# Optimization experiments

Hardware: AMD Instinct MI355X
Metric: run time of the kernel (lower is better)

The kernel has to match this reference:

```python
import jax, jax.numpy as jnp
import numpy as np

C_M, C_Z, H, CH = 256, 128, 8, 32
EPS = 1e-5

def layer_norm(x, g, b):
    mu = jnp.mean(x, axis=-1, keepdims=True)
    var = jnp.mean(jnp.square(x - mu), axis=-1, keepdims=True)
    return (x - mu) * jax.lax.rsqrt(var + EPS) * g + b

def setup_inputs() -> dict:
    key = jax.random.key(0)
    ks = jax.random.split(key, 12)
    B, N, L = 1, 256, 256
    m = jax.random.normal(ks[0], (B, N, L, C_M), dtype=jnp.float32)
    z = jax.random.normal(ks[1], (B, L, L, C_Z), dtype=jnp.float32)
    msa_mask = jax.random.randint(ks[2], (B, N, L), 0, 2, dtype=jnp.int32)
    s = 0.02
    return {
        "m": m, "z": z, "msa_mask": msa_mask,
        "ln_m_g": jnp.ones((C_M,), jnp.float32), "ln_m_b": jnp.zeros((C_M,), jnp.float32),
        "ln_z_g": jnp.ones((C_Z,), jnp.float32), "ln_z_b": jnp.zeros((C_Z,), jnp.float32),
        "Wq": s * jax.random.normal(ks[3], (C_M, H * CH), jnp.float32),
        "Wk": s * jax.random.normal(ks[4], (C_M, H * CH), jnp.float32),
        "Wv": s * jax.random.normal(ks[5], (C_M, H * CH), jnp.float32),
        "Wb": s * jax.random.normal(ks[6], (C_Z, H), jnp.float32),
        "Wg": s * jax.random.normal(ks[7], (C_M, H * CH), jnp.float32),
        "bg": jnp.zeros((H * CH,), jnp.float32),
        "Wo": s * jax.random.normal(ks[8], (H * CH, C_M), jnp.float32),
        "bo": jnp.zeros((C_M,), jnp.float32),
    }

def reference(m, z, msa_mask, ln_m_g, ln_m_b, ln_z_g, ln_z_b,
              Wq, Wk, Wv, Wb, Wg, bg, Wo, bo):
    B, N, L, _ = m.shape
    mn = layer_norm(m, ln_m_g, ln_m_b)          # [B,N,L,c_m]
    zn = layer_norm(z, ln_z_g, ln_z_b)          # [B,L,L,c_z]
    q = (mn @ Wq).reshape(B, N, L, H, CH)
    k = (mn @ Wk).reshape(B, N, L, H, CH)
    v = (mn @ Wv).reshape(B, N, L, H, CH)
    pair_bias = zn @ Wb                          # [B,L,L,H]
    logits = jnp.einsum('bnihc,bnjhc->bnhij', q, k) / np.sqrt(CH).astype(np.float32)
    logits = logits + jnp.transpose(pair_bias, (0, 3, 1, 2))[:, None]  # [B,1,H,i,j]
    # key mask over j: [B,N,1,1,L]
    logits = jnp.where(msa_mask[:, :, None, None, :] == 0, jnp.float32(-1e9), logits)
    attn = jax.nn.softmax(logits, axis=-1)
    out = jnp.einsum('bnhij,bnjhc->bnihc', attn, v)
    gate = jax.nn.sigmoid(mn @ Wg + bg).reshape(B, N, L, H, CH)
    out = (out * gate).reshape(B, N, L, H * CH)
    out = out @ Wo + bo
    out = out * msa_mask[..., None].astype(out.dtype)
    return out
```

## Files before the change

### kernel.cpp

```cpp
#include <hip/hip_runtime.h>

typedef unsigned short ushort_t;
typedef unsigned int uint_t;
typedef __attribute__((ext_vector_type(8))) short bf16x8;
typedef __attribute__((ext_vector_type(4))) float f32x4;

#define EPSV 1e-5f
#define LOG2E 1.4426950408889634f
#define QSC (0.17677669529663687f * LOG2E)

__device__ __forceinline__ float u2f(uint_t x) { return __builtin_bit_cast(float, x); }
__device__ __forceinline__ uint_t f2u(float x) { return __builtin_bit_cast(uint_t, x); }
__device__ __forceinline__ float bflo(uint_t u) { return u2f(u << 16); }
__device__ __forceinline__ float bfhi(uint_t u) { return u2f(u & 0xFFFF0000u); }
__device__ __forceinline__ ushort_t f2bf(float f) {
    uint_t x = f2u(f);
    x += 0x7FFFu + ((x >> 16) & 1u);
    return (ushort_t)(x >> 16);
}
__device__ __forceinline__ uint_t cvtpk(float lo, float hi) {
    uint_t r;
    asm("v_cvt_pk_bf16_f32 %0, %1, %2" : "=v"(r) : "v"(lo), "v"(hi));
    return r;
}
__device__ __forceinline__ float exp2v(float x) {
    float r;
    asm("v_exp_f32 %0, %1" : "=v"(r) : "v"(x));
    return r;
}
__device__ __forceinline__ float rcpv(float x) {
    float r;
    asm("v_rcp_f32 %0, %1" : "=v"(r) : "v"(x));
    return r;
}
__device__ __forceinline__ f32x4 mfma16(bf16x8 a, bf16x8 b, f32x4 c) {
    return __builtin_amdgcn_mfma_f32_16x16x32_bf16(a, b, c, 0, 0, 0);
}
__device__ __forceinline__ float wsum(float v) {
#pragma unroll
    for (int m = 32; m >= 1; m >>= 1) v += __shfl_xor(v, m, 64);
    return v;
}

#define NB_LN 16384
#define NB_PB 1024
__global__ __launch_bounds__(256) void k_pre(const float* __restrict__ m,
                                             const float* __restrict__ ln_m_g,
                                             const float* __restrict__ ln_m_b,
                                             const float* __restrict__ z,
                                             const float* __restrict__ ln_z_g,
                                             const float* __restrict__ ln_z_b,
                                             const float* __restrict__ Wb,
                                             const float* __restrict__ Wq, const float* __restrict__ Wk,
                                             const float* __restrict__ Wv, const float* __restrict__ Wg,
                                             const float* __restrict__ Wo,
                                             ushort_t* __restrict__ mn,
                                             float* __restrict__ pb,
                                             ushort_t* __restrict__ wtT, ushort_t* __restrict__ woT) {
    __shared__ float wb_lds[1024];
    const int bid = blockIdx.x, t = threadIdx.x;

    if (bid < NB_LN) {
        const int lane = t & 63;
        const int row  = bid * 4 + (t >> 6);
        const float4 x = *(const float4*)(m + (size_t)row * 256 + lane * 4);
        const float mu = wsum(x.x + x.y + x.z + x.w) * (1.f / 256.f);
        const float dx = x.x - mu, dy = x.y - mu, dz = x.z - mu, dw = x.w - mu;
        const float var = wsum(dx * dx + dy * dy + dz * dz + dw * dw) * (1.f / 256.f);
        const float rs = rsqrtf(var + EPSV);
        const float4 gg = *(const float4*)(ln_m_g + lane * 4);
        const float4 bb = *(const float4*)(ln_m_b + lane * 4);
        ushort4 o;
        o.x = f2bf(dx * rs * gg.x + bb.x);
        o.y = f2bf(dy * rs * gg.y + bb.y);
        o.z = f2bf(dz * rs * gg.z + bb.z);
        o.w = f2bf(dw * rs * gg.w + bb.w);
        *(ushort4*)(mn + (size_t)row * 256 + lane * 4) = o;
    } else if (bid < NB_LN + NB_PB) {
        const int pbid = bid - NB_LN;
        const int w = t >> 6, l = t & 63;
        const int l16 = l & 15, gq = l >> 4;
        *(float4*)&wb_lds[t * 4] = *(const float4*)(Wb + t * 4);
        __syncthreads();

        const int row = pbid * 64 + w * 16 + l16;
        const float* zr = z + (size_t)row * 128;
        float v[32];
        float s1 = 0.f, s2 = 0.f;
#pragma unroll
        for (int ks = 0; ks < 4; ++ks) {
            const float4 a0 = *(const float4*)(zr + ks * 32 + gq * 8);
            const float4 a1 = *(const float4*)(zr + ks * 32 + gq * 8 + 4);
            v[ks * 8 + 0] = a0.x; v[ks * 8 + 1] = a0.y; v[ks * 8 + 2] = a0.z; v[ks * 8 + 3] = a0.w;
            v[ks * 8 + 4] = a1.x; v[ks * 8 + 5] = a1.y; v[ks * 8 + 6] = a1.z; v[ks * 8 + 7] = a1.w;
        }
#pragma unroll
        for (int j = 0; j < 32; ++j) { s1 += v[j]; s2 += v[j] * v[j]; }
        s1 += __shfl_xor(s1, 16, 64); s1 += __shfl_xor(s1, 32, 64);
        s2 += __shfl_xor(s2, 16, 64); s2 += __shfl_xor(s2, 32, 64);
        const float mu = s1 * (1.f / 128.f);
        const float var = s2 * (1.f / 128.f) - mu * mu;
        const float rs = rsqrtf(var + EPSV);

        f32x4 acc = (f32x4){0.f, 0.f, 0.f, 0.f};
#pragma unroll
        for (int ks = 0; ks < 4; ++ks) {
            const float4 g0 = *(const float4*)(ln_z_g + ks * 32 + gq * 8);
            const float4 g1 = *(const float4*)(ln_z_g + ks * 32 + gq * 8 + 4);
            const float4 b0 = *(const float4*)(ln_z_b + ks * 32 + gq * 8);
            const float4 b1 = *(const float4*)(ln_z_b + ks * 32 + gq * 8 + 4);
            const float xn0 = (v[ks * 8 + 0] - mu) * rs * g0.x + b0.x;
            const float xn1 = (v[ks * 8 + 1] - mu) * rs * g0.y + b0.y;
            const float xn2 = (v[ks * 8 + 2] - mu) * rs * g0.z + b0.z;
            const float xn3 = (v[ks * 8 + 3] - mu) * rs * g0.w + b0.w;
            const float xn4 = (v[ks * 8 + 4] - mu) * rs * g1.x + b1.x;
            const float xn5 = (v[ks * 8 + 5] - mu) * rs * g1.y + b1.y;
            const float xn6 = (v[ks * 8 + 6] - mu) * rs * g1.z + b1.z;
            const float xn7 = (v[ks * 8 + 7] - mu) * rs * g1.w + b1.w;
            uint4 pk;
            pk.x = cvtpk(xn0, xn1); pk.y = cvtpk(xn2, xn3);
            pk.z = cvtpk(xn4, xn5); pk.w = cvtpk(xn6, xn7);
            const bf16x8 af = __builtin_bit_cast(bf16x8, pk);
            ushort_t wf[8];
#pragma unroll
            for (int j = 0; j < 8; ++j)
                wf[j] = (l16 < 8) ? f2bf(wb_lds[(ks * 32 + gq * 8 + j) * 8 + l16]) : (ushort_t)0;
            const bf16x8 bf_ = *(const bf16x8*)wf;
            acc = mfma16(af, bf_, acc);
        }
        if (l16 < 8) {
            const int orow = pbid * 64 + w * 16 + gq * 4;
            f32x4 o;
            o[0] = acc[0] * LOG2E; o[1] = acc[1] * LOG2E;
            o[2] = acc[2] * LOG2E; o[3] = acc[3] * LOG2E;
            *(f32x4*)(pb + (size_t)l16 * 65536 + orow) = o;
        }
    } else {
        const int k = bid - (NB_LN + NB_PB);
        const int h = t >> 5, c = t & 31;
        wtT[(size_t)(h * 128 +   0 + c) * 256 + k] = f2bf(Wq[k * 256 + t]);
        wtT[(size_t)(h * 128 +  32 + c) * 256 + k] = f2bf(Wk[k * 256 + t]);
        wtT[(size_t)(h * 128 +  64 + c) * 256 + k] = f2bf(Wv[k * 256 + t]);
        wtT[(size_t)(h * 128 +  96 + c) * 256 + k] = f2bf(Wg[k * 256 + t]);
        woT[(size_t)t * 256 + k] = f2bf(Wo[k * 256 + t]);
    }
}

__global__ __launch_bounds__(256, 1) void k_attn(const ushort_t* __restrict__ mn,
                                                 const ushort_t* __restrict__ wtT,
                                                 const float* __restrict__ pb,
                                                 const int* __restrict__ msa_mask,
                                                 const float* __restrict__ bg,
                                                 ushort_t* __restrict__ ao) {
    __shared__ ushort_t k_s[256 * 40];
    __shared__ ushort_t qp_s[256 * 40];
    __shared__ ushort_t vT[32 * 264];
    __shared__ ushort_t gT[32 * 264];
    __shared__ float maskb[256];

    const int t = threadIdx.x;
    const int n = blockIdx.x & 255, h = blockIdx.x >> 8;
    const int w = t >> 6, l = t & 63;
    const int l16 = l & 15, g = l >> 4;

    maskb[t] = msa_mask[n * 256 + t] ? 0.f : -1.5e9f;
    const float bg0 = bg[h * 32 + l16];
    const float bg1 = bg[h * 32 + 16 + l16];

    const ushort_t* mb = mn + (size_t)n * 65536;
    const ushort_t* wb = wtT + (size_t)h * 128 * 256;

#pragma unroll
    for (int chalf = 0; chalf < 2; ++chalf) {
        f32x4 acc[4][4];
#pragma unroll
        for (int rt = 0; rt < 4; ++rt)
#pragma unroll
            for (int ct = 0; ct < 4; ++ct) acc[rt][ct] = (f32x4){0.f, 0.f, 0.f, 0.f};

#pragma unroll
        for (int ks = 0; ks < 8; ++ks) {
            bf16x8 a[4], b[4];
#pragma unroll
            for (int rt = 0; rt < 4; ++rt)
                a[rt] = *(const bf16x8*)(mb + (size_t)(w * 64 + rt * 16 + l16) * 256 + ks * 32 + g * 8);
#pragma unroll
            for (int ct = 0; ct < 4; ++ct)
                b[ct] = *(const bf16x8*)(wb + (size_t)(chalf * 64 + ct * 16 + l16) * 256 + ks * 32 + g * 8);
#pragma unroll
            for (int rt = 0; rt < 4; ++rt)
#pragma unroll
                for (int ct = 0; ct < 4; ++ct)
                    acc[rt][ct] = mfma16(a[rt], b[ct], acc[rt][ct]);
        }
#pragma unroll
        for (int ct = 0; ct < 4; ++ct) {
            const int mat = chalf * 2 + (ct >> 1);
            const int cc = (ct & 1) * 16 + l16;
#pragma unroll
            for (int rt = 0; rt < 4; ++rt) {
                const int i0 = w * 64 + rt * 16 + g * 4;
                const f32x4 v = acc[rt][ct];
                if (mat == 0) {
#pragma unroll
                    for (int r = 0; r < 4; ++r) qp_s[(i0 + r) * 40 + cc] = f2bf(v[r] * QSC);
                } else if (mat == 1) {
#pragma unroll
                    for (int r = 0; r < 4; ++r) k_s[(i0 + r) * 40 + cc] = f2bf(v[r]);
                } else if (mat == 2) {
                    const uint_t lo = cvtpk(v[0], v[1]);
                    const uint_t hi = cvtpk(v[2], v[3]);
                    *(uint2*)(vT + cc * 264 + i0) = make_uint2(lo, hi);
                } else {
                    const float bgc = (ct & 1) ? bg1 : bg0;
                    float gt[4];
#pragma unroll
                    for (int r = 0; r < 4; ++r)
                        gt[r] = rcpv(1.f + exp2v(-(v[r] + bgc) * LOG2E));
                    const uint_t lo = cvtpk(gt[0], gt[1]);
                    const uint_t hi = cvtpk(gt[2], gt[3]);
                    *(uint2*)(gT + cc * 264 + i0) = make_uint2(lo, hi);
                }
            }
        }
    }
    __syncthreads();

    bf16x8 bq[4];
#pragma unroll
    for (int it = 0; it < 4; ++it)
        bq[it] = *(const bf16x8*)&qp_s[(w * 64 + it * 16 + l16) * 40 + g * 8];
    ushort_t* p_w = qp_s + w * 64 * 40;

    const float* pbh = pb + (size_t)h * 65536;
    f32x4 oT[2][4];
#pragma unroll
    for (int ct = 0; ct < 2; ++ct)
#pragma unroll
        for (int it = 0; it < 4; ++it) oT[ct][it] = (f32x4){0.f, 0.f, 0.f, 0.f};
    float lsum[4] = {0.f, 0.f, 0.f, 0.f};

    bf16x8 ak[2], av[2];
    f32x4 pc0[4], pc1[4];
#pragma unroll
    for (int jt = 0; jt < 2; ++jt)
        ak[jt] = *(const bf16x8*)&k_s[(jt * 16 + l16) * 40 + g * 8];
#pragma unroll
    for (int ct = 0; ct < 2; ++ct)
        av[ct] = *(const bf16x8*)&vT[(ct * 16 + l16) * 264 + g * 8];
#pragma unroll
    for (int it = 0; it < 4; ++it) {
        const int i = w * 64 + it * 16 + l16;
        pc0[it] = *(const f32x4*)(pbh + (size_t)i * 256 + g * 4);
        pc1[it] = *(const f32x4*)(pbh + (size_t)i * 256 + 16 + g * 4);
    }

    for (int jc = 0; jc < 8; ++jc) {
        bf16x8 akn[2], avn[2];
        f32x4 pn0[4], pn1[4];
        if (jc < 7) {
            const int j0 = (jc + 1) * 32;
#pragma unroll
            for (int jt = 0; jt < 2; ++jt)
                akn[jt] = *(const bf16x8*)&k_s[(j0 + jt * 16 + l16) * 40 + g * 8];
#pragma unroll
            for (int ct = 0; ct < 2; ++ct)
                avn[ct] = *(const bf16x8*)&vT[(ct * 16 + l16) * 264 + j0 + g * 8];
#pragma unroll
            for (int it = 0; it < 4; ++it) {
                const int i = w * 64 + it * 16 + l16;
                pn0[it] = *(const f32x4*)(pbh + (size_t)i * 256 + j0 + g * 4);
                pn1[it] = *(const f32x4*)(pbh + (size_t)i * 256 + j0 + 16 + g * 4);
            }
        }

        f32x4 st[2][4];
        __builtin_amdgcn_s_setprio(1);
#pragma unroll
        for (int jt = 0; jt < 2; ++jt)
#pragma unroll
            for (int it = 0; it < 4; ++it)
                st[jt][it] = mfma16(ak[jt], bq[it], (f32x4){0.f, 0.f, 0.f, 0.f});
        __builtin_amdgcn_s_setprio(0);

        const f32x4 mk0 = *(const f32x4*)&maskb[jc * 32 + g * 4];
        const f32x4 mk1 = *(const f32x4*)&maskb[jc * 32 + 16 + g * 4];

#pragma unroll
        for (int it = 0; it < 4; ++it) {
            float p0[4], p1[4];
#pragma unroll
            for (int r = 0; r < 4; ++r) {
                p0[r] = exp2v(st[0][it][r] + pc0[it][r] + mk0[r]);
                p1[r] = exp2v(st[1][it][r] + pc1[it][r] + mk1[r]);
            }
#pragma unroll
            for (int r = 0; r < 4; ++r) lsum[it] += p0[r] + p1[r];
            ushort_t* base = p_w + (it * 16 + l16) * 40;
            *(uint2*)(base + g * 4)      = make_uint2(cvtpk(p0[0], p0[1]), cvtpk(p0[2], p0[3]));
            *(uint2*)(base + 16 + g * 4) = make_uint2(cvtpk(p1[0], p1[1]), cvtpk(p1[2], p1[3]));
        }
        __builtin_amdgcn_s_setprio(1);
#pragma unroll
        for (int it = 0; it < 4; ++it) {
            const bf16x8 bp = *(const bf16x8*)&p_w[(it * 16 + l16) * 40 + g * 8];
            oT[0][it] = mfma16(av[0], bp, oT[0][it]);
            oT[1][it] = mfma16(av[1], bp, oT[1][it]);
        }
        __builtin_amdgcn_s_setprio(0);

        if (jc < 7) {
#pragma unroll
            for (int jt = 0; jt < 2; ++jt) ak[jt] = akn[jt];
#pragma unroll
            for (int ct = 0; ct < 2; ++ct) av[ct] = avn[ct];
#pragma unroll
            for (int it = 0; it < 4; ++it) { pc0[it] = pn0[it]; pc1[it] = pn1[it]; }
        }
    }

    float inv[4];
#pragma unroll
    for (int it = 0; it < 4; ++it) {
        float s = lsum[it];
        s += __shfl_xor(s, 16, 64);
        s += __shfl_xor(s, 32, 64);
        inv[it] = rcpv(s);
    }

    __syncthreads();
    ushort_t* oT_s = vT;
#pragma unroll
    for (int ct = 0; ct < 2; ++ct)
#pragma unroll
        for (int it = 0; it < 4; ++it) {
            const int i = w * 64 + it * 16 + l16;
#pragma unroll
            for (int r = 0; r < 4; ++r) {
                const int c = ct * 16 + g * 4 + r;
                const float gate = bflo((uint_t)gT[c * 264 + i]);
                oT_s[c * 264 + i] = f2bf(oT[ct][it][r] * inv[it] * gate);
            }
        }
    __syncthreads();
    ushort_t* aob = ao + (size_t)n * 256 * 256 + h * 32;
#pragma unroll
    for (int iter = 0; iter < 16; ++iter) {
        const int flat = iter * 256 + t;
        const int i = flat >> 4, cp = flat & 15;
        const uint_t lo = oT_s[(2 * cp) * 264 + i];
        const uint_t hi = oT_s[(2 * cp + 1) * 264 + i];
        *(uint_t*)(aob + (size_t)i * 256 + 2 * cp) = lo | (hi << 16);
    }
}

__global__ __launch_bounds__(256, 2) void k_out(const ushort_t* __restrict__ ao,
                                                const ushort_t* __restrict__ woT,
                                                const float* __restrict__ bo,
                                                const int* __restrict__ msa_mask,
                                                float* __restrict__ out) {
    const int t = threadIdx.x;
    const int rb = blockIdx.x * 128;
    const int w = t >> 6, l = t & 63;
    const int l16 = l & 15, g = l >> 4;

#pragma unroll
    for (int ch = 0; ch < 2; ++ch) {
        f32x4 acc[2][8];
#pragma unroll
        for (int rt = 0; rt < 2; ++rt)
#pragma unroll
            for (int ct = 0; ct < 8; ++ct) acc[rt][ct] = (f32x4){0.f, 0.f, 0.f, 0.f};
#pragma unroll
        for (int ks = 0; ks < 8; ++ks) {
            bf16x8 a[2], b[8];
#pragma unroll
            for (int rt = 0; rt < 2; ++rt)
                a[rt] = *(const bf16x8*)(ao + (size_t)(rb + w * 32 + rt * 16 + l16) * 256 + ks * 32 + g * 8);
#pragma unroll
            for (int ct = 0; ct < 8; ++ct)
                b[ct] = *(const bf16x8*)(woT + (size_t)(ch * 128 + ct * 16 + l16) * 256 + ks * 32 + g * 8);
#pragma unroll
            for (int rt = 0; rt < 2; ++rt)
#pragma unroll
                for (int ct = 0; ct < 8; ++ct)
                    acc[rt][ct] = mfma16(a[rt], b[ct], acc[rt][ct]);
        }
#pragma unroll
        for (int rt = 0; rt < 2; ++rt)
#pragma unroll
            for (int ct = 0; ct < 8; ++ct) {
                const int c = ch * 128 + ct * 16 + l16;
                const float boc = bo[c];
#pragma unroll
                for (int r = 0; r < 4; ++r) {
                    const int row = rb + w * 32 + rt * 16 + g * 4 + r;
                    const float mk = msa_mask[row] ? 1.f : 0.f;
                    out[(size_t)row * 256 + c] = (acc[rt][ct][r] + boc) * mk;
                }
            }
    }
}

extern "C" void kernel_launch(void* const* d_in, const int* in_sizes, int n_in,
                              void* d_out, int out_size, void* d_ws, size_t ws_size,
                              hipStream_t stream) {
    const float* m       = (const float*)d_in[0];
    const float* z       = (const float*)d_in[1];
    const int* msa_mask  = (const int*)d_in[2];
    const float* ln_m_g  = (const float*)d_in[3];
    const float* ln_m_b  = (const float*)d_in[4];
    const float* ln_z_g  = (const float*)d_in[5];
    const float* ln_z_b  = (const float*)d_in[6];
    const float* Wq      = (const float*)d_in[7];
    const float* Wk      = (const float*)d_in[8];
    const float* Wv      = (const float*)d_in[9];
    const float* Wb      = (const float*)d_in[10];
    const float* Wg      = (const float*)d_in[11];
    const float* bg      = (const float*)d_in[12];
    const float* Wo      = (const float*)d_in[13];
    const float* bo      = (const float*)d_in[14];
    float* out           = (float*)d_out;

    char* ws = (char*)d_ws;
    ushort_t* mn  = (ushort_t*)(ws);
    float*    pb  = (float*)(ws + 33554432);
    ushort_t* ao  = (ushort_t*)(ws + 35651584);
    ushort_t* wtT = (ushort_t*)(ws + 69206016);
    ushort_t* woT = (ushort_t*)(ws + 69730304);

    k_pre<<<17664, 256, 0, stream>>>(m, ln_m_g, ln_m_b, z, ln_z_g, ln_z_b, Wb,
                                     Wq, Wk, Wv, Wg, Wo, mn, pb, wtT, woT);
    k_attn<<<2048, 256, 0, stream>>>(mn, wtT, pb, msa_mask, bg, ao);
    k_out<<<512, 256, 0, stream>>>(ao, woT, bo, msa_mask, out);
}
```

Before: 262.5 us.

## Swizzle attention LDS tiles and keep gate values in registers

Replaces the padded shared-memory layouts for Q/P, K and transposed V with unpadded XOR-swizzled layouts, so rows pack densely while bank conflicts stay low. The sigmoid gate is kept packed in registers during the attention loop instead of in its own LDS buffer. It is written into the freed Q/P buffer only at the end, and the gated output is staged through the K buffer. This cuts per-block LDS use, which may allow more resident blocks per CU, at the cost of extra address arithmetic and more live registers.

```diff
diff --git a/kernel.cpp b/kernel.cpp
--- a/kernel.cpp
+++ b/kernel.cpp
@@ -40,6 +40,12 @@
 #pragma unroll
     for (int m = 32; m >= 1; m >>= 1) v += __shfl_xor(v, m, 64);
     return v;
+}
+__device__ __forceinline__ int swz32(int row, int col) {
+    return (row * 32 + col) ^ ((row & 7) << 3);
+}
+__device__ __forceinline__ int swzT(int c, int i) {
+    return c * 256 + (i ^ ((c & 7) << 3));
 }
 
 #define NB_LN 16384
@@ -152,10 +158,9 @@
                                                  const int* __restrict__ msa_mask,
                                                  const float* __restrict__ bg,
                                                  ushort_t* __restrict__ ao) {
-    __shared__ ushort_t k_s[256 * 40];
-    __shared__ ushort_t qp_s[256 * 40];
-    __shared__ ushort_t vT[32 * 264];
-    __shared__ ushort_t gT[32 * 264];
+    __shared__ ushort_t k_s[8192];
+    __shared__ ushort_t qp_s[8192];
+    __shared__ ushort_t vT_s[8192];
     __shared__ float maskb[256];
 
     const int t = threadIdx.x;
@@ -170,6 +175,8 @@
     const ushort_t* mb = mn + (size_t)n * 65536;
     const ushort_t* wb = wtT + (size_t)h * 128 * 256;
 
+    uint2 gpk[2][4];
+
 #pragma unroll
     for (int chalf = 0; chalf < 2; ++chalf) {
         f32x4 acc[4][4];
@@ -203,23 +210,19 @@
                 const f32x4 v = acc[rt][ct];
                 if (mat == 0) {
 #pragma unroll
-                    for (int r = 0; r < 4; ++r) qp_s[(i0 + r) * 40 + cc] = f2bf(v[r] * QSC);
+                    for (int r = 0; r < 4; ++r) qp_s[swz32(i0 + r, cc)] = f2bf(v[r] * QSC);
                 } else if (mat == 1) {
 #pragma unroll
-                    for (int r = 0; r < 4; ++r) k_s[(i0 + r) * 40 + cc] = f2bf(v[r]);
+                    for (int r = 0; r < 4; ++r) k_s[swz32(i0 + r, cc)] = f2bf(v[r]);
                 } else if (mat == 2) {
-                    const uint_t lo = cvtpk(v[0], v[1]);
-                    const uint_t hi = cvtpk(v[2], v[3]);
-                    *(uint2*)(vT + cc * 264 + i0) = make_uint2(lo, hi);
+                    *(uint2*)&vT_s[swzT(cc, i0)] = make_uint2(cvtpk(v[0], v[1]), cvtpk(v[2], v[3]));
                 } else {
                     const float bgc = (ct & 1) ? bg1 : bg0;
                     float gt[4];
 #pragma unroll
                     for (int r = 0; r < 4; ++r)
                         gt[r] = rcpv(1.f + exp2v(-(v[r] + bgc) * LOG2E));
-                    const uint_t lo = cvtpk(gt[0], gt[1]);
-                    const uint_t hi = cvtpk(gt[2], gt[3]);
-                    *(uint2*)(gT + cc * 264 + i0) = make_uint2(lo, hi);
+                    gpk[ct & 1][rt] = make_uint2(cvtpk(gt[0], gt[1]), cvtpk(gt[2], gt[3]));
                 }
             }
         }
@@ -229,8 +232,7 @@
     bf16x8 bq[4];
 #pragma unroll
     for (int it = 0; it < 4; ++it)
-        bq[it] = *(const bf16x8*)&qp_s[(w * 64 + it * 16 + l16) * 40 + g * 8];
-    ushort_t* p_w = qp_s + w * 64 * 40;
+        bq[it] = *(const bf16x8*)&qp_s[swz32(w * 64 + it * 16 + l16, g * 8)];
 
     const float* pbh = pb + (size_t)h * 65536;
     f32x4 oT[2][4];
@@ -244,10 +246,10 @@
     f32x4 pc0[4], pc1[4];
 #pragma unroll
     for (int jt = 0; jt < 2; ++jt)
-        ak[jt] = *(const bf16x8*)&k_s[(jt * 16 + l16) * 40 + g * 8];
+        ak[jt] = *(const bf16x8*)&k_s[swz32(jt * 16 + l16, g * 8)];
 #pragma unroll
     for (int ct = 0; ct < 2; ++ct)
-        av[ct] = *(const bf16x8*)&vT[(ct * 16 + l16) * 264 + g * 8];
+        av[ct] = *(const bf16x8*)&vT_s[swzT(ct * 16 + l16, g * 8)];
 #pragma unroll
     for (int it = 0; it < 4; ++it) {
         const int i = w * 64 + it * 16 + l16;
@@ -262,10 +264,10 @@
             const int j0 = (jc + 1) * 32;
 #pragma unroll
             for (int jt = 0; jt < 2; ++jt)
-                akn[jt] = *(const bf16x8*)&k_s[(j0 + jt * 16 + l16) * 40 + g * 8];
+                akn[jt] = *(const bf16x8*)&k_s[swz32(j0 + jt * 16 + l16, g * 8)];
 #pragma unroll
             for (int ct = 0; ct < 2; ++ct)
-                avn[ct] = *(const bf16x8*)&vT[(ct * 16 + l16) * 264 + j0 + g * 8];
+                avn[ct] = *(const bf16x8*)&vT_s[swzT(ct * 16 + l16, j0 + g * 8)];
 #pragma unroll
             for (int it = 0; it < 4; ++it) {
                 const int i = w * 64 + it * 16 + l16;
@@ -296,14 +298,14 @@
             }
 #pragma unroll
             for (int r = 0; r < 4; ++r) lsum[it] += p0[r] + p1[r];
-            ushort_t* base = p_w + (it * 16 + l16) * 40;
-            *(uint2*)(base + g * 4)      = make_uint2(cvtpk(p0[0], p0[1]), cvtpk(p0[2], p0[3]));
-            *(uint2*)(base + 16 + g * 4) = make_uint2(cvtpk(p1[0], p1[1]), cvtpk(p1[2], p1[3]));
+            const int row = w * 64 + it * 16 + l16;
+            *(uint2*)&qp_s[swz32(row, g * 4)]      = make_uint2(cvtpk(p0[0], p0[1]), cvtpk(p0[2], p0[3]));
+            *(uint2*)&qp_s[swz32(row, 16 + g * 4)] = make_uint2(cvtpk(p1[0], p1[1]), cvtpk(p1[2], p1[3]));
         }
         __builtin_amdgcn_s_setprio(1);
 #pragma unroll
         for (int it = 0; it < 4; ++it) {
-            const bf16x8 bp = *(const bf16x8*)&p_w[(it * 16 + l16) * 40 + g * 8];
+            const bf16x8 bp = *(const bf16x8*)&qp_s[swz32(w * 64 + it * 16 + l16, g * 8)];
             oT[0][it] = mfma16(av[0], bp, oT[0][it]);
             oT[1][it] = mfma16(av[1], bp, oT[1][it]);
         }
@@ -329,7 +331,16 @@
     }
 
     __syncthreads();
-    ushort_t* oT_s = vT;
+
+#pragma unroll
+    for (int ct = 0; ct < 2; ++ct) {
+        const int cc = ct * 16 + l16;
+#pragma unroll
+        for (int rt = 0; rt < 4; ++rt) {
+            const int i0 = w * 64 + rt * 16 + g * 4;
+            *(uint2*)&qp_s[swzT(cc, i0)] = gpk[ct][rt];
+        }
+    }
 #pragma unroll
     for (int ct = 0; ct < 2; ++ct)
 #pragma unroll
@@ -338,8 +349,8 @@
 #pragma unroll
             for (int r = 0; r < 4; ++r) {
                 const int c = ct * 16 + g * 4 + r;
-                const float gate = bflo((uint_t)gT[c * 264 + i]);
-                oT_s[c * 264 + i] = f2bf(oT[ct][it][r] * inv[it] * gate);
+                const float gate = bflo((uint_t)qp_s[swzT(c, i)]);
+                k_s[swzT(c, i)] = f2bf(oT[ct][it][r] * inv[it] * gate);
             }
         }
     __syncthreads();
@@ -348,8 +359,8 @@
     for (int iter = 0; iter < 16; ++iter) {
         const int flat = iter * 256 + t;
         const int i = flat >> 4, cp = flat & 15;
-        const uint_t lo = oT_s[(2 * cp) * 264 + i];
-        const uint_t hi = oT_s[(2 * cp + 1) * 264 + i];
+        const uint_t lo = k_s[swzT(2 * cp, i)];
+        const uint_t hi = k_s[swzT(2 * cp + 1, i)];
         *(uint_t*)(aob + (size_t)i * 256 + 2 * cp) = lo | (hi << 16);
     }
 }
```

Result: slower. 291.5 us (+11.0%).
